# Kernel optimization log

Measured on AMD Instinct MI355X. Metric: run time of the kernel, lower is better.

The kernel has to match this reference:

```python
import jax, jax.numpy as jnp
import numpy as np

B, L, V, E, D, NH, HD, NL = 4, 2048, 32000, 300, 128, 4, 128, 3
D2 = NH * HD  # 512
W = 3  # ring window size (unfold_size)
EPS = 1e-5


def setup_inputs() -> dict:
    key = jax.random.key(0)
    ks = jax.random.split(key, 16)
    s = 0.02
    w = lambda k, shape: (jax.random.normal(k, shape, jnp.float32) * s)
    inp = {
        "tokens": jax.random.randint(ks[0], (B, L), 0, V),
        "mask": jax.random.randint(ks[1], (B, L), 0, 2).astype(jnp.int32),
        "emb_table": w(ks[2], (V, E)),
        "proj_w": w(ks[3], (D, E)),
        "proj_b": jnp.zeros((D,), jnp.float32),
        "ng": jnp.ones((NL, D), jnp.float32),
        "nb": jnp.zeros((NL, D), jnp.float32),
        "rq_w": w(ks[4], (NL, D2, D)), "rq_b": jnp.zeros((NL, D2), jnp.float32),
        "rk_w": w(ks[5], (NL, D2, D)), "rk_b": jnp.zeros((NL, D2), jnp.float32),
        "rv_w": w(ks[6], (NL, D2, D)), "rv_b": jnp.zeros((NL, D2), jnp.float32),
        "ro_w": w(ks[7], (NL, D, D2)), "ro_b": jnp.zeros((NL, D), jnp.float32),
        "sq_w": w(ks[8], (NL, D2, D)), "sq_b": jnp.zeros((NL, D2), jnp.float32),
        "sk_w": w(ks[9], (NL, D2, D)), "sk_b": jnp.zeros((NL, D2), jnp.float32),
        "sv_w": w(ks[10], (NL, D2, D)), "sv_b": jnp.zeros((NL, D2), jnp.float32),
        "so_w": w(ks[11], (NL, D, D2)), "so_b": jnp.zeros((NL, D), jnp.float32),
    }
    return inp


def _layernorm(x, g, b):
    mu = x.mean(-1, keepdims=True)
    var = x.var(-1, keepdims=True)
    return (x - mu) / jnp.sqrt(var + EPS) * g + b


def reference(tokens, mask, emb_table, proj_w, proj_b, ng, nb,
              rq_w, rq_b, rk_w, rk_b, rv_w, rv_b, ro_w, ro_b,
              sq_w, sq_b, sk_w, sk_b, sv_w, sv_b, so_w, so_b):
    b, l = tokens.shape
    pad = (mask == 0)                                        # [B,L] True at padding
    smask = jnp.concatenate([jnp.zeros((b, 1), bool), pad], axis=1)  # [B,L+1]
    x = emb_table[tokens] @ proj_w.T + proj_b                # [B,L,D]
    nodes = x
    relay = x.mean(axis=1)                                   # [B,D]
    r_embs = x                                               # fixed original embeddings
    scale = 1.0 / np.sqrt(HD).astype(np.float32)
    for i in range(NL):
        nx = _layernorm(nodes, ng[i], nb[i])
        # ----- MSA1: ring (windowed) attention + relay extras -----
        q = (nx @ rq_w[i].T + rq_b[i]).reshape(b, l, NH, HD)
        k = (nx @ rk_w[i].T + rk_b[i]).reshape(b, l, NH, HD)
        v = (nx @ rv_w[i].T + rv_b[i]).reshape(b, l, NH, HD)
        relay_bc = jnp.broadcast_to(relay[:, None, :], (b, l, D))
        ax = jnp.stack([r_embs, relay_bc], axis=2)           # [B,L,2,D]
        ak = (ax @ rk_w[i].T + rk_b[i]).reshape(b, l, 2, NH, HD)
        av = (ax @ rv_w[i].T + rv_b[i]).reshape(b, l, 2, NH, HD)
        kp = jnp.pad(k, ((0, 0), (1, 1), (0, 0), (0, 0)))    # zero pad like F.unfold
        vp = jnp.pad(v, ((0, 0), (1, 1), (0, 0), (0, 0)))
        kw = jnp.stack([kp[:, u:u + l] for u in range(W)], axis=2)  # [B,L,3,NH,HD]
        vw = jnp.stack([vp[:, u:u + l] for u in range(W)], axis=2)
        kall = jnp.concatenate([kw, ak], axis=2)             # [B,L,5,NH,HD]
        vall = jnp.concatenate([vw, av], axis=2)
        scores = jnp.einsum('blnh,blunh->blun', q, kall) * scale
        alphas = jax.nn.softmax(scores, axis=2)
        att = jnp.einsum('blun,blunh->blnh', alphas, vall).reshape(b, l, D2)
        nodes = nodes + jax.nn.leaky_relu(att @ ro_w[i].T + ro_b[i])
        # ----- MSA2: relay (global) attention over [relay; nodes] -----
        y = jnp.concatenate([relay[:, None, :], nodes], axis=1)      # [B,L+1,D]
        sq = (relay @ sq_w[i].T + sq_b[i]).reshape(b, NH, HD)
        sk = (y @ sk_w[i].T + sk_b[i]).reshape(b, l + 1, NH, HD)
        sv = (y @ sv_w[i].T + sv_b[i]).reshape(b, l + 1, NH, HD)
        pre = jnp.einsum('bnh,blnh->bnl', sq, sk) * scale            # [B,NH,L+1]
        pre = jnp.where(smask[:, None, :], -jnp.inf, pre)
        al = jax.nn.softmax(pre, axis=2)
        satt = jnp.einsum('bnl,blnh->bnh', al, sv).reshape(b, D2)
        relay = jax.nn.leaky_relu(satt @ so_w[i].T + so_b[i])
        nodes = jnp.where(pad[:, :, None], 0.0, nodes)
    return relay  # a_v: [B, d_model] (use_attention=False path)
```

## Files before the change

### kernel.cpp

```cpp
#include <hip/hip_runtime.h>
#include <hip/hip_bf16.h>

constexpr int B = 4, L = 2048, E = 300, D = 128, NH = 4, HD = 128, NL = 3, D2 = 512;
constexpr float EPS = 1e-5f;
constexpr float SCALE = 0.08838834764831843f;
constexpr int NCH = 64;

typedef unsigned int uint_t;
typedef unsigned short u16;
typedef short bf16x8 __attribute__((ext_vector_type(8)));
typedef float f32x4 __attribute__((ext_vector_type(4)));

__device__ __forceinline__ u16 f2bf(float f) {
  union { float f; uint_t i; } x; x.f = f;
  uint_t r = x.i + 0x7fffu + ((x.i >> 16) & 1u);
  return (u16)(r >> 16);
}
__device__ __forceinline__ uint_t packbf(float a, float b) {
  return (uint_t)f2bf(a) | ((uint_t)f2bf(b) << 16);
}
__device__ __forceinline__ float bf2f(u16 u) {
  union { uint_t i; float f; } x; x.i = ((uint_t)u) << 16; return x.f;
}
__device__ __forceinline__ float2 bf2x2(uint_t u) {
  union { uint_t i; float f; } a, b;
  a.i = (u & 0xffffu) << 16; b.i = u & 0xffff0000u;
  return make_float2(a.f, b.f);
}
struct f8 { float v[8]; };
__device__ __forceinline__ f8 unpack8(uint4 u) {
  f8 r;
  float2 a = bf2x2(u.x); r.v[0] = a.x; r.v[1] = a.y;
  float2 b = bf2x2(u.y); r.v[2] = b.x; r.v[3] = b.y;
  float2 c = bf2x2(u.z); r.v[4] = c.x; r.v[5] = c.y;
  float2 d = bf2x2(u.w); r.v[6] = d.x; r.v[7] = d.y;
  return r;
}

struct WCArgs { const float* s[4]; u16* d[4]; };
__global__ __launch_bounds__(256) void wconv(WCArgs wa) {
  int ti = blockIdx.y;
  const float* s = wa.s[ti]; u16* dd = wa.d[ti];
  int i = (blockIdx.x * 256 + threadIdx.x) * 4;
  float4 f = *(const float4*)(s + i);
  *(uint2*)(dd + i) = make_uint2(packbf(f.x, f.y), packbf(f.z, f.w));
}

struct GDesc { const u16* A; const u16* W; const float* bias; u16* outb; };
struct GArgs { GDesc d[5]; };

__global__ __launch_bounds__(256) void gemm_qkv(GArgs ga, int nby, int N) {
  __shared__ u16 As[128][136];
  __shared__ u16 Ws[128][136];
  int t = threadIdx.x;
  int bm = blockIdx.x;
  int di = blockIdx.y / nby, bn = blockIdx.y - di * nby;
  GDesc d = ga.d[di];
  const int rowA = bm * 128, rowW = bn * 128;

  f32x4 acc[4][4];
#pragma unroll
  for (int i = 0; i < 4; i++)
#pragma unroll
    for (int j = 0; j < 4; j++)
      acc[i][j] = (f32x4){0.f, 0.f, 0.f, 0.f};

  const int r = t >> 1, c0 = (t & 1) * 64;
  const int wid = t >> 6;
  const int wm = (wid & 1) * 64, wn = (wid >> 1) * 64;
  const int lr = t & 15, quad = (t >> 4) & 3;

  const u16* Arow = d.A + (size_t)(rowA + r) * 128;
  const u16* Wrow = d.W + (size_t)(rowW + r) * 128;
  uint4 av_[8], wv_[8];
#pragma unroll
  for (int i = 0; i < 8; i++) {
    av_[i] = *(const uint4*)(Arow + c0 + i * 8);
    wv_[i] = *(const uint4*)(Wrow + c0 + i * 8);
  }
#pragma unroll
  for (int i = 0; i < 8; i++) {
    *(uint4*)&As[r][c0 + i * 8] = av_[i];
    *(uint4*)&Ws[r][c0 + i * 8] = wv_[i];
  }
  __syncthreads();
#pragma unroll
  for (int ks = 0; ks < 4; ks++) {
    bf16x8 af[4], bfr[4];
#pragma unroll
    for (int mt = 0; mt < 4; mt++)
      af[mt] = *(const bf16x8*)&As[wm + mt * 16 + lr][ks * 32 + quad * 8];
#pragma unroll
    for (int nt = 0; nt < 4; nt++)
      bfr[nt] = *(const bf16x8*)&Ws[wn + nt * 16 + lr][ks * 32 + quad * 8];
#pragma unroll
    for (int mt = 0; mt < 4; mt++)
#pragma unroll
      for (int nt = 0; nt < 4; nt++)
        acc[mt][nt] = __builtin_amdgcn_mfma_f32_16x16x32_bf16(af[mt], bfr[nt], acc[mt][nt], 0, 0, 0);
  }
  __syncthreads();
#pragma unroll
  for (int nt = 0; nt < 4; nt++) {
    int colL = wn + nt * 16 + lr;
    float bv = d.bias[rowW + colL];
#pragma unroll
    for (int mt = 0; mt < 4; mt++) {
#pragma unroll
      for (int rr = 0; rr < 4; rr++) {
        int rowL = wm + mt * 16 + quad * 4 + rr;
        As[rowL][colL] = f2bf(acc[mt][nt][rr] + bv);
      }
    }
  }
  __syncthreads();
#pragma unroll
  for (int rep = 0; rep < 8; rep++) {
    int lin = rep * 256 + t;
    int rowL = lin >> 4, colL = (lin & 15) * 8;
    uint4 v = *(const uint4*)&As[rowL][colL];
    *(uint4*)&d.outb[(size_t)(rowA + rowL) * N + rowW + colL] = v;
  }
}

__global__ __launch_bounds__(256) void gemm_embed_ln(
    const float* __restrict__ emb, const float* __restrict__ W,
    const float* __restrict__ bias, const int* __restrict__ gather,
    const float* __restrict__ lng, const float* __restrict__ lnb,
    float* __restrict__ nodes, u16* __restrict__ xb, u16* __restrict__ nxb,
    float* __restrict__ relay) {
  __shared__ u16 As[64][72];
  __shared__ u16 Ws[128][72];
  __shared__ float C[64][132];
  __shared__ float gb[2][D];
  __shared__ float lmu[64], lrs[64];
  int t = threadIdx.x;
  int bm = blockIdx.x;
  const int rowA0 = bm * 64;

  f32x4 acc[2][4];
#pragma unroll
  for (int i = 0; i < 2; i++)
#pragma unroll
    for (int j = 0; j < 4; j++)
      acc[i][j] = (f32x4){0.f, 0.f, 0.f, 0.f};

  const int wid = t >> 6;
  const int wm = (wid & 1) * 32, wn = (wid >> 1) * 64;
  const int lr = t & 15, quad = (t >> 4) & 3;
  const int ra = t >> 2, ca = (t & 3) * 16;
  const int rw = t >> 1, cw = (t & 1) * 32;

  if (t < D) { gb[0][t] = lng[t]; gb[1][t] = lnb[t]; }

  const float* Arow = emb + (size_t)gather[rowA0 + ra] * E;
  const float* Wrow = W + (size_t)rw * E;

  for (int kt = 0; kt < E; kt += 64) {
    __syncthreads();
    bool full = (kt + 64 <= E);
#pragma unroll
    for (int ch = 0; ch < 4; ch++) {
      int c = kt + ca + ch * 4;
      float4 fa;
      if (full) fa = *(const float4*)(Arow + c);
      else {
        fa.x = (c + 0 < E) ? Arow[c + 0] : 0.f;
        fa.y = (c + 1 < E) ? Arow[c + 1] : 0.f;
        fa.z = (c + 2 < E) ? Arow[c + 2] : 0.f;
        fa.w = (c + 3 < E) ? Arow[c + 3] : 0.f;
      }
      *(uint2*)&As[ra][ca + ch * 4] = make_uint2(packbf(fa.x, fa.y), packbf(fa.z, fa.w));
    }
#pragma unroll
    for (int ch = 0; ch < 8; ch++) {
      int c = kt + cw + ch * 4;
      float4 fw;
      if (full) fw = *(const float4*)(Wrow + c);
      else {
        fw.x = (c + 0 < E) ? Wrow[c + 0] : 0.f;
        fw.y = (c + 1 < E) ? Wrow[c + 1] : 0.f;
        fw.z = (c + 2 < E) ? Wrow[c + 2] : 0.f;
        fw.w = (c + 3 < E) ? Wrow[c + 3] : 0.f;
      }
      *(uint2*)&Ws[rw][cw + ch * 4] = make_uint2(packbf(fw.x, fw.y), packbf(fw.z, fw.w));
    }
    __syncthreads();
#pragma unroll
    for (int ks = 0; ks < 2; ks++) {
      bf16x8 af[2], bfr[4];
#pragma unroll
      for (int mt = 0; mt < 2; mt++)
        af[mt] = *(const bf16x8*)&As[wm + mt * 16 + lr][ks * 32 + quad * 8];
#pragma unroll
      for (int nt = 0; nt < 4; nt++)
        bfr[nt] = *(const bf16x8*)&Ws[wn + nt * 16 + lr][ks * 32 + quad * 8];
#pragma unroll
      for (int mt = 0; mt < 2; mt++)
#pragma unroll
        for (int nt = 0; nt < 4; nt++)
          acc[mt][nt] = __builtin_amdgcn_mfma_f32_16x16x32_bf16(af[mt], bfr[nt], acc[mt][nt], 0, 0, 0);
    }
  }
#pragma unroll
  for (int nt = 0; nt < 4; nt++) {
    int col = wn + nt * 16 + lr;
    float bv = bias[col];
#pragma unroll
    for (int mt = 0; mt < 2; mt++) {
#pragma unroll
      for (int rr = 0; rr < 4; rr++) {
        int row = wm + mt * 16 + quad * 4 + rr;
        C[row][col] = acc[mt][nt][rr] + bv;
      }
    }
  }
  __syncthreads();
  if (t < 64) {
    float s = 0.f, s2 = 0.f;
#pragma unroll 16
    for (int j = 0; j < D; j++) { float v = C[t][j]; s += v; s2 += v * v; }
    float mu = s * (1.0f / D);
    float var = s2 * (1.0f / D) - mu * mu;
    lmu[t] = mu; lrs[t] = rsqrtf(var + EPS);
  }
  __syncthreads();
#pragma unroll
  for (int rep = 0; rep < 8; rep++) {
    int lin = rep * 1024 + t * 4;
    int row = lin >> 7, col = lin & 127;
    float4 v = *(const float4*)&C[row][col];
    size_t g = (size_t)(rowA0 + row) * D + col;
    *(float4*)&nodes[g] = v;
    *(uint2*)&xb[g] = make_uint2(packbf(v.x, v.y), packbf(v.z, v.w));
    float mu = lmu[row], rs = lrs[row];
    float o0 = (v.x - mu) * rs * gb[0][col] + gb[1][col];
    float o1 = (v.y - mu) * rs * gb[0][col + 1] + gb[1][col + 1];
    float o2 = (v.z - mu) * rs * gb[0][col + 2] + gb[1][col + 2];
    float o3 = (v.w - mu) * rs * gb[0][col + 3] + gb[1][col + 3];
    *(uint2*)&nxb[g] = make_uint2(packbf(o0, o1), packbf(o2, o3));
  }
  if (t < D) {
    int b = rowA0 >> 11;
    float s = 0.f;
#pragma unroll 16
    for (int r2 = 0; r2 < 64; r2++) s += C[r2][t];
    atomicAdd(&relay[b * D + t], s * (1.0f / L));
  }
}

__global__ __launch_bounds__(256) void gemm_ro_ln(
    const u16* __restrict__ A,
    const u16* __restrict__ W,
    const float* __restrict__ bias,
    const int* __restrict__ mask,
    const float* __restrict__ lng, const float* __restrict__ lnb,
    const float* __restrict__ uvec, const float* __restrict__ cvec,
    float* __restrict__ nodes, u16* __restrict__ nxb,
    float* __restrict__ pm, float* __restrict__ ps, float* __restrict__ pw,
    int do_ln) {
  __shared__ u16 As[32][136];
  __shared__ u16 Ws[128][136];
  __shared__ float C[32][132];
  __shared__ float gb[2][D];
  __shared__ float lmu[32], lrs[32];
  __shared__ float usv[NH][D];
  __shared__ float cv2[NH];
  __shared__ float scs[NH][32];
  __shared__ float esr[NH][32];
  int t = threadIdx.x;
  int bm = blockIdx.x;
  const int rowA0 = bm * 32;
  const int b4 = rowA0 >> 11;
  const int chunk = (rowA0 >> 5) & 63;

  f32x4 acc[4];
#pragma unroll
  for (int j = 0; j < 4; j++) acc[j] = (f32x4){0.f, 0.f, 0.f, 0.f};

  const int wid = t >> 6;
  const int wm = (wid & 1) * 16, wn = (wid >> 1) * 64;
  const int lr = t & 15, quad = (t >> 4) & 3;
  const int ra = t >> 3, ca = (t & 7) * 16;
  const int rw = t >> 1, cw = (t & 1) * 64;

  if (do_ln && t < D) { gb[0][t] = lng[t]; gb[1][t] = lnb[t]; }
#pragma unroll
  for (int rep = 0; rep < 2; rep++) {
    int idx = rep * 256 + t;
    usv[idx >> 7][idx & 127] = uvec[(size_t)b4 * NH * D + idx];
  }
  if (t < NH) cv2[t] = cvec[b4 * NH + t];

  const u16* Arow = A + (size_t)(rowA0 + ra) * 512;
  const u16* Wrow = W + (size_t)rw * 512;

  for (int kt = 0; kt < 512; kt += 128) {
    uint4 a0 = *(const uint4*)(Arow + kt + ca);
    uint4 a1 = *(const uint4*)(Arow + kt + ca + 8);
    uint4 w0 = *(const uint4*)(Wrow + kt + cw);
    uint4 w1 = *(const uint4*)(Wrow + kt + cw + 8);
    uint4 w2 = *(const uint4*)(Wrow + kt + cw + 16);
    uint4 w3 = *(const uint4*)(Wrow + kt + cw + 24);
    uint4 w4 = *(const uint4*)(Wrow + kt + cw + 32);
    uint4 w5 = *(const uint4*)(Wrow + kt + cw + 40);
    uint4 w6 = *(const uint4*)(Wrow + kt + cw + 48);
    uint4 w7 = *(const uint4*)(Wrow + kt + cw + 56);
    __syncthreads();
    *(uint4*)&As[ra][ca] = a0; *(uint4*)&As[ra][ca + 8] = a1;
    *(uint4*)&Ws[rw][cw] = w0; *(uint4*)&Ws[rw][cw + 8] = w1;
    *(uint4*)&Ws[rw][cw + 16] = w2; *(uint4*)&Ws[rw][cw + 24] = w3;
    *(uint4*)&Ws[rw][cw + 32] = w4; *(uint4*)&Ws[rw][cw + 40] = w5;
    *(uint4*)&Ws[rw][cw + 48] = w6; *(uint4*)&Ws[rw][cw + 56] = w7;
    __syncthreads();
#pragma unroll
    for (int ks = 0; ks < 4; ks++) {
      bf16x8 af = *(const bf16x8*)&As[wm + lr][ks * 32 + quad * 8];
      bf16x8 bfr[4];
#pragma unroll
      for (int nt = 0; nt < 4; nt++)
        bfr[nt] = *(const bf16x8*)&Ws[wn + nt * 16 + lr][ks * 32 + quad * 8];
#pragma unroll
      for (int nt = 0; nt < 4; nt++)
        acc[nt] = __builtin_amdgcn_mfma_f32_16x16x32_bf16(af, bfr[nt], acc[nt], 0, 0, 0);
    }
  }
  __syncthreads();
#pragma unroll
  for (int nt = 0; nt < 4; nt++) {
    int col = wn + nt * 16 + lr;
    float bv = bias[col];
#pragma unroll
    for (int rr = 0; rr < 4; rr++) {
      int row = wm + quad * 4 + rr;
      float v = acc[nt][rr] + bv;
      v = (v > 0.f) ? v : 0.01f * v;
      v += nodes[(size_t)(rowA0 + row) * D + col];
      if (mask[rowA0 + row] == 0) v = 0.f;
      C[row][col] = v;
    }
  }
  __syncthreads();
  if (t < 32) {
    float s = 0.f, s2 = 0.f;
#pragma unroll 16
    for (int j = 0; j < D; j++) { float v = C[t][j]; s += v; s2 += v * v; }
    float mu = s * (1.0f / D);
    float var = s2 * (1.0f / D) - mu * mu;
    lmu[t] = mu; lrs[t] = rsqrtf(var + EPS);
  }
  __syncthreads();
#pragma unroll
  for (int rep = 0; rep < 4; rep++) {
    int lin = rep * 1024 + t * 4;
    int row = lin >> 7, col = lin & 127;
    float4 v = *(const float4*)&C[row][col];
    size_t g = (size_t)(rowA0 + row) * D + col;
    *(float4*)&nodes[g] = v;
    if (do_ln) {
      float mu = lmu[row], rs = lrs[row];
      float o0 = (v.x - mu) * rs * gb[0][col] + gb[1][col];
      float o1 = (v.y - mu) * rs * gb[0][col + 1] + gb[1][col + 1];
      float o2 = (v.z - mu) * rs * gb[0][col + 2] + gb[1][col + 2];
      float o3 = (v.w - mu) * rs * gb[0][col + 3] + gb[1][col + 3];
      *(uint2*)&nxb[g] = make_uint2(packbf(o0, o1), packbf(o2, o3));
    }
  }
  {
    int n = wid, lane = t & 63;
    int bn = b4 * NH + n;
    const float2* un = (const float2*)usv[n];
    float2 uv2 = un[lane];
    for (int r2 = 0; r2 < 32; r2++) {
      float2 cc = ((const float2*)&C[r2][0])[lane];
      float p = uv2.x * cc.x + uv2.y * cc.y;
#pragma unroll
      for (int o = 1; o < 64; o <<= 1) p += __shfl_xor(p, o, 64);
      if (lane == 0) {
        float s = p + cv2[n];
        if (mask[rowA0 + r2] == 0) s = -1e30f;
        scs[n][r2] = s;
      }
    }
    float m = -1e30f;
    for (int r2 = 0; r2 < 32; r2++) m = fmaxf(m, scs[n][r2]);
    if (lane < 32) esr[n][lane] = expf(scs[n][lane] - m);
    float sum = 0.f;
    for (int r2 = 0; r2 < 32; r2++) sum += esr[n][r2];
    if (lane == 0) { pm[bn * NCH + chunk] = m; ps[bn * NCH + chunk] = sum; }
    float a0 = 0.f, a1 = 0.f;
    for (int r2 = 0; r2 < 32; r2++) {
      float e = esr[n][r2];
      float2 cc = ((const float2*)&C[r2][0])[lane];
      a0 += e * cc.x; a1 += e * cc.y;
    }
    float* pwp = pw + ((size_t)bn * NCH + chunk) * D + 2 * lane;
    pwp[0] = a0; pwp[1] = a1;
  }
}

__device__ __forceinline__ void do_relay_proj(
    int b, int di, int t, const float* rel,
    const float* rkw, const float* rkb, const float* rvw, const float* rvb,
    const float* sqw, const float* sqb, const float* skw, const float* skb_,
    float* relay_k, float* relay_v, float* u, float* cvec,
    float* sql, float* cred) {
  const float4* r4 = (const float4*)rel;
  if (di < 8) {
    int which = di >> 2;
    int n = (di & 3) * 128 + t;
    const float* W = which ? rvw : rkw;
    float acc = (which ? rvb : rkb)[n];
    const float4* w4 = (const float4*)(W + (size_t)n * D);
#pragma unroll 8
    for (int i = 0; i < D / 4; i++) {
      float4 w = w4[i], r = r4[i];
      acc += w.x * r.x + w.y * r.y + w.z * r.z + w.w * r.w;
    }
    (which ? relay_v : relay_k)[(size_t)b * D2 + n] = acc;
  } else {
    int n = di - 8;
    {
      int nh = n * HD + t;
      float acc = sqb[nh];
      const float4* w4 = (const float4*)(sqw + (size_t)nh * D);
#pragma unroll 8
      for (int i = 0; i < D / 4; i++) {
        float4 w = w4[i], r = r4[i];
        acc += w.x * r.x + w.y * r.y + w.z * r.z + w.w * r.w;
      }
      sql[t] = acc;
    }
    __syncthreads();
    {
      float cp = sql[t] * skb_[n * HD + t];
#pragma unroll
      for (int o = 1; o < 64; o <<= 1) cp += __shfl_xor(cp, o, 64);
      if ((t & 63) == 0) cred[t >> 6] = cp;
    }
    float a0 = 0.f, a1 = 0.f, a2 = 0.f, a3 = 0.f;
    const float* wp = skw + (size_t)(n * HD) * D + t;
    for (int h = 0; h < HD; h += 4) {
      a0 += sql[h] * wp[(size_t)h * D];
      a1 += sql[h + 1] * wp[(size_t)(h + 1) * D];
      a2 += sql[h + 2] * wp[(size_t)(h + 2) * D];
      a3 += sql[h + 3] * wp[(size_t)(h + 3) * D];
    }
    u[((size_t)b * NH + n) * D + t] = (a0 + a1 + a2 + a3) * SCALE;
    __syncthreads();
    if (t == 0) cvec[b * NH + n] = (cred[0] + cred[1]) * SCALE;
  }
}

__global__ __launch_bounds__(128) void relay_proj(
    const float* __restrict__ relay,
    const float* __restrict__ rkw, const float* __restrict__ rkb,
    const float* __restrict__ rvw, const float* __restrict__ rvb,
    const float* __restrict__ sqw, const float* __restrict__ sqb,
    const float* __restrict__ skw, const float* __restrict__ skb_,
    float* __restrict__ relay_k, float* __restrict__ relay_v,
    float* __restrict__ u, float* __restrict__ cvec) {
  __shared__ float rel[D];
  __shared__ float sql[HD];
  __shared__ float cred[2];
  int b = blockIdx.x, di = blockIdx.y, t = threadIdx.x;
  rel[t] = relay[(size_t)b * D + t];
  __syncthreads();
  do_relay_proj(b, di, t, rel, rkw, rkb, rvw, rvb, sqw, sqb, skw, skb_,
                relay_k, relay_v, u, cvec, sql, cred);
}

__global__ __launch_bounds__(256) void ring_attn_kernel(
    const u16* __restrict__ q, const u16* __restrict__ k, const u16* __restrict__ v,
    const u16* __restrict__ akr, const u16* __restrict__ avr,
    const float* __restrict__ rk, const float* __restrict__ rv,
    u16* __restrict__ att) {
  int wv = threadIdx.x >> 6, lane = threadIdx.x & 63;
  int bl = blockIdx.x * 4 + wv;
  int b = bl >> 11, l = bl & (L - 1);
  size_t rowoff = (size_t)bl * D2 + lane * 8;

  uint4 qd = *(const uint4*)(q + rowoff);
  uint4 kd[5], vd[5];
  bool valid[3];
#pragma unroll
  for (int u = 0; u < 3; u++) {
    int ll = l + u - 1;
    valid[u] = (ll >= 0 && ll < L);
    size_t off = ((size_t)b * L + ll) * D2 + lane * 8;
    if (valid[u]) { kd[u] = *(const uint4*)(k + off); vd[u] = *(const uint4*)(v + off); }
    else { kd[u] = make_uint4(0, 0, 0, 0); vd[u] = make_uint4(0, 0, 0, 0); }
  }
  kd[3] = *(const uint4*)(akr + rowoff);
  vd[3] = *(const uint4*)(avr + rowoff);
  size_t rb = (size_t)b * D2 + lane * 8;
  float4 rk0 = *(const float4*)(rk + rb), rk1 = *(const float4*)(rk + rb + 4);
  float4 rv0 = *(const float4*)(rv + rb), rv1 = *(const float4*)(rv + rb + 4);

  f8 qf = unpack8(qd);
  f8 kf[5], vf[5];
#pragma unroll
  for (int u = 0; u < 4; u++) { kf[u] = unpack8(kd[u]); vf[u] = unpack8(vd[u]); }
  kf[4].v[0] = rk0.x; kf[4].v[1] = rk0.y; kf[4].v[2] = rk0.z; kf[4].v[3] = rk0.w;
  kf[4].v[4] = rk1.x; kf[4].v[5] = rk1.y; kf[4].v[6] = rk1.z; kf[4].v[7] = rk1.w;
  vf[4].v[0] = rv0.x; vf[4].v[1] = rv0.y; vf[4].v[2] = rv0.z; vf[4].v[3] = rv0.w;
  vf[4].v[4] = rv1.x; vf[4].v[5] = rv1.y; vf[4].v[6] = rv1.z; vf[4].v[7] = rv1.w;

  float s[5];
#pragma unroll
  for (int u = 0; u < 5; u++) {
    float p = 0.f;
#pragma unroll
    for (int j = 0; j < 8; j++) p += qf.v[j] * kf[u].v[j];
#pragma unroll
    for (int o = 1; o < 16; o <<= 1) p += __shfl_xor(p, o, 64);
    s[u] = p * SCALE;
  }
  float m = s[0];
#pragma unroll
  for (int u = 1; u < 5; u++) m = fmaxf(m, s[u]);
  float e[5], sum = 0.f;
#pragma unroll
  for (int u = 0; u < 5; u++) { e[u] = expf(s[u] - m); sum += e[u]; }
  float inv = 1.0f / sum;
  float o[8];
#pragma unroll
  for (int j = 0; j < 8; j++) {
    float a = 0.f;
#pragma unroll
    for (int u = 0; u < 5; u++) a += e[u] * vf[u].v[j];
    o[j] = a * inv;
  }
  uint4 od;
  od.x = packbf(o[0], o[1]); od.y = packbf(o[2], o[3]);
  od.z = packbf(o[4], o[5]); od.w = packbf(o[6], o[7]);
  *(uint4*)(att + rowoff) = od;
}

__global__ __launch_bounds__(128) void relay_final(
    const float* __restrict__ pm, const float* __restrict__ ps, const float* __restrict__ pw,
    const float* __restrict__ relay_entry,
    const float* __restrict__ uvec_in, const float* __restrict__ cvec_in,
    const float* __restrict__ svw, const float* __restrict__ svb,
    const float* __restrict__ sow, const float* __restrict__ sob,
    const float* __restrict__ nrkw, const float* __restrict__ nrkb,
    const float* __restrict__ nrvw, const float* __restrict__ nrvb,
    const float* __restrict__ nsqw, const float* __restrict__ nsqb,
    const float* __restrict__ nskw, const float* __restrict__ nskb,
    float* __restrict__ relay_out,
    float* __restrict__ relay_k, float* __restrict__ relay_v,
    float* __restrict__ u_out, float* __restrict__ cvec_out, int do_proj) {
  int b = blockIdx.x, di = blockIdx.y, t = threadIdx.x;
  __shared__ float uu[NH][D];
  __shared__ float rel0[D];
  __shared__ float pms[NH][NCH], pss[NH][NCH], ecs[NH][NCH];
  __shared__ float s0s[NH], cvs[NH];
  __shared__ float wsum[NH][D];
  __shared__ float satts[D2];
  __shared__ float rel[D];
  __shared__ float sql[HD];
  __shared__ float cred[2];

  rel0[t] = relay_entry[(size_t)b * D + t];
#pragma unroll
  for (int rep = 0; rep < 4; rep++) {
    int idx = rep * 128 + t;
    uu[idx >> 7][idx & 127] = uvec_in[(size_t)b * NH * D + idx];
  }
  if (t < NH) cvs[t] = cvec_in[b * NH + t];
#pragma unroll
  for (int rep = 0; rep < 2; rep++) {
    int idx = rep * 128 + t;
    int n = idx >> 6, c = idx & 63;
    pms[n][c] = pm[(b * NH + n) * NCH + c];
    pss[n][c] = ps[(b * NH + n) * NCH + c];
  }
  __syncthreads();
  int g = t >> 5, lt = t & 31;
  {
    float p = 0.f;
#pragma unroll
    for (int kk = 0; kk < 4; kk++) { int j = lt * 4 + kk; p += uu[g][j] * rel0[j]; }
#pragma unroll
    for (int o = 1; o < 32; o <<= 1) p += __shfl_xor(p, o, 64);
    if (lt == 0) s0s[g] = p + cvs[g];
  }
  __syncthreads();
  float s0 = s0s[g];
  float M = s0;
  for (int c = 0; c < NCH; c++) M = fmaxf(M, pms[g][c]);
  for (int c = lt; c < NCH; c += 32) ecs[g][c] = expf(pms[g][c] - M);
  __syncthreads();
  float e0 = expf(s0 - M);
  float S = e0;
  for (int c = 0; c < NCH; c++) S += pss[g][c] * ecs[g][c];
  float invS = 1.0f / S;
#pragma unroll
  for (int kk = 0; kk < 4; kk++) {
    int h = lt * 4 + kk;
    float acc = e0 * rel0[h];
    const float* pwp = pw + ((size_t)(b * NH + g) * NCH) * D + h;
    for (int c = 0; c < NCH; c++) acc += ecs[g][c] * pwp[(size_t)c * D];
    wsum[g][h] = acc * invS;
  }
  __syncthreads();
#pragma unroll
  for (int rep = 0; rep < 4; rep++) {
    int nh = rep * 128 + t;
    int hn = nh >> 7;
    float acc = svb[nh];
    const float4* wp = (const float4*)(svw + (size_t)nh * D);
    const float4* wl = (const float4*)wsum[hn];
#pragma unroll 8
    for (int d = 0; d < D / 4; d++) {
      float4 a = wl[d], wv4 = wp[d];
      acc += a.x * wv4.x + a.y * wv4.y + a.z * wv4.z + a.w * wv4.w;
    }
    satts[nh] = acc;
  }
  __syncthreads();
  {
    float acc = sob[t];
    const float4* wp = (const float4*)(sow + (size_t)t * D2);
    const float4* a4 = (const float4*)satts;
#pragma unroll 8
    for (int j = 0; j < D2 / 4; j++) {
      float4 a = a4[j], wv4 = wp[j];
      acc += a.x * wv4.x + a.y * wv4.y + a.z * wv4.z + a.w * wv4.w;
    }
    acc = (acc > 0.f) ? acc : 0.01f * acc;
    rel[t] = acc;
    relay_out[(size_t)b * D + t] = acc;
  }
  __syncthreads();
  if (do_proj)
    do_relay_proj(b, di, t, rel, nrkw, nrkb, nrvw, nrvb, nsqw, nsqb, nskw, nskb,
                  relay_k, relay_v, u_out, cvec_out, sql, cred);
}

extern "C" void kernel_launch(void* const* d_in, const int* in_sizes, int n_in,
                              void* d_out, int out_size, void* d_ws, size_t ws_size,
                              hipStream_t stream) {
  const int* tokens = (const int*)d_in[0];
  const int* mask = (const int*)d_in[1];
  const float* emb = (const float*)d_in[2];
  const float* proj_w = (const float*)d_in[3];
  const float* proj_b = (const float*)d_in[4];
  const float* ng = (const float*)d_in[5];
  const float* nb = (const float*)d_in[6];
  const float* rq_w = (const float*)d_in[7], * rq_b = (const float*)d_in[8];
  const float* rk_w = (const float*)d_in[9], * rk_b = (const float*)d_in[10];
  const float* rv_w = (const float*)d_in[11], * rv_b = (const float*)d_in[12];
  const float* ro_w = (const float*)d_in[13], * ro_b = (const float*)d_in[14];
  const float* sq_w = (const float*)d_in[15], * sq_b = (const float*)d_in[16];
  const float* sk_w = (const float*)d_in[17], * sk_b = (const float*)d_in[18];
  const float* sv_w = (const float*)d_in[19], * sv_b = (const float*)d_in[20];
  const float* so_w = (const float*)d_in[21], * so_b = (const float*)d_in[22];

  const size_t BLD = (size_t)B * L * D;
  const size_t BLD4 = (size_t)B * L * D2;
  const size_t WTEN = (size_t)NL * D * D2;

  float* fp = (float*)d_ws;
  float* nodes = fp;                    fp += BLD;
  float* rbuf0 = fp;                    fp += B * D;
  float* rbuf1 = fp;                    fp += B * D;
  float* relay_k = fp;                  fp += B * D2;
  float* relay_v = fp;                  fp += B * D2;
  float* uv0 = fp;                      fp += B * NH * D;
  float* uv1 = fp;                      fp += B * NH * D;
  float* cv0 = fp;                      fp += B * NH;
  float* cv1 = fp;                      fp += B * NH;
  float* pm = fp;                       fp += B * NH * NCH;
  float* ps = fp;                       fp += B * NH * NCH;
  float* pw = fp;                       fp += (size_t)B * NH * NCH * D;
  u16* up = (u16*)fp;
  u16* xb = up;                         up += BLD;
  u16* nxb = up;                        up += BLD;
  u16* qb = up;                         up += BLD4;
  u16* kb = up;                         up += BLD4;
  u16* vb = up;                         up += BLD4;
  u16* akb = up;                        up += BLD4;
  u16* avb = up;                        up += BLD4;
  u16* attb = up;                       up += BLD4;
  u16* wb = up;
  u16* wrq = wb, * wrk = wb + WTEN, * wrv = wb + 2 * WTEN, * wro = wb + 3 * WTEN;

  float* rbuf[2] = {rbuf0, rbuf1};
  float* uv[2] = {uv0, uv1};
  float* cv[2] = {cv0, cv1};

  hipMemsetAsync(rbuf0, 0, B * D * sizeof(float), stream);

  {
    WCArgs wa;
    wa.s[0] = rq_w; wa.s[1] = rk_w; wa.s[2] = rv_w; wa.s[3] = ro_w;
    wa.d[0] = wrq; wa.d[1] = wrk; wa.d[2] = wrv; wa.d[3] = wro;
    wconv<<<dim3(WTEN / 1024, 4), 256, 0, stream>>>(wa);
  }
  gemm_embed_ln<<<128, 256, 0, stream>>>(emb, proj_w, proj_b, tokens, ng, nb,
                                         nodes, xb, nxb, rbuf0);
  relay_proj<<<dim3(B, 12), 128, 0, stream>>>(rbuf0, rk_w, rk_b, rv_w, rv_b, sq_w, sq_b,
                                              sk_w, sk_b, relay_k, relay_v, uv0, cv0);

  for (int i = 0; i < NL; i++) {
    const size_t wo = (size_t)i * D * D2;
    const float* rqbi = rq_b + (size_t)i * D2;
    const float* rkbi = rk_b + (size_t)i * D2;
    const float* rvbi = rv_b + (size_t)i * D2;
    const float* robi = ro_b + (size_t)i * D;
    const float* svwi = sv_w + wo, * svbi = sv_b + (size_t)i * D2;
    const float* sowi = so_w + wo, * sobi = so_b + (size_t)i * D;
    const int e = i & 1, nx2 = e ^ 1;
    const int last = (i == NL - 1);

    {
      GArgs ga = {};
      ga.d[0] = {nxb, wrq + wo, rqbi, qb};
      ga.d[1] = {nxb, wrk + wo, rkbi, kb};
      ga.d[2] = {nxb, wrv + wo, rvbi, vb};
      ga.d[3] = {xb,  wrk + wo, rkbi, akb};
      ga.d[4] = {xb,  wrv + wo, rvbi, avb};
      gemm_qkv<<<dim3(64, 20), 256, 0, stream>>>(ga, 4, D2);
    }
    ring_attn_kernel<<<B * L / 4, 256, 0, stream>>>(qb, kb, vb, akb, avb, relay_k, relay_v, attb);
    gemm_ro_ln<<<256, 256, 0, stream>>>(
        attb, wro + wo, robi, mask,
        last ? nullptr : ng + (i + 1) * D, last ? nullptr : nb + (i + 1) * D,
        uv[e], cv[e], nodes, nxb, pm, ps, pw, last ? 0 : 1);
    const size_t wn_ = (size_t)(i + 1) * D * D2;
    float* relay_dst = last ? (float*)d_out : rbuf[nx2];
    relay_final<<<dim3(B, last ? 1 : 12), 128, 0, stream>>>(
        pm, ps, pw, rbuf[e], uv[e], cv[e], svwi, svbi, sowi, sobi,
        last ? nullptr : rk_w + wn_, last ? nullptr : rk_b + (size_t)(i + 1) * D2,
        last ? nullptr : rv_w + wn_, last ? nullptr : rv_b + (size_t)(i + 1) * D2,
        last ? nullptr : sq_w + wn_, last ? nullptr : sq_b + (size_t)(i + 1) * D2,
        last ? nullptr : sk_w + wn_, last ? nullptr : sk_b + (size_t)(i + 1) * D2,
        relay_dst, relay_k, relay_v, uv[nx2], cv[nx2], last ? 0 : 1);
  }
}
```

Before: 387.5 us.

## Fold relay projections into QKV GEMM launch and slim relay combine kernel

Moves the per-layer relay key/value/query projection work out of the relay-final kernel and the initial standalone launch, and runs it as 24 extra blocks prepended to the QKV GEMM grid. The relay combine kernel becomes a single 512-thread block per batch with wider parallel reductions, and no longer holds the projection stage serially at its tail. The aim is to remove one kernel launch plus a serialized low-parallelism tail per layer by overlapping the small projections with the GEMM. The u/c buffers are no longer double-buffered, which relies on stream ordering between the combine kernel and the next GEMM.

Result: faster. 361.4 us (-6.7%).

```diff
diff --git a/kernel.cpp b/kernel.cpp
--- a/kernel.cpp
+++ b/kernel.cpp
@@ -48,13 +48,77 @@
 
 struct GDesc { const u16* A; const u16* W; const float* bias; u16* outb; };
 struct GArgs { GDesc d[5]; };
-
-__global__ __launch_bounds__(256) void gemm_qkv(GArgs ga, int nby, int N) {
+struct PArgs {
+  const float* rel;
+  const float* rkw; const float* rkb;
+  const float* rvw; const float* rvb;
+  const float* sqw; const float* sqb;
+  const float* skw; const float* skb;
+  float* relay_k; float* relay_v;
+  float* u; float* cvec;
+};
+constexpr int NPROJ = 24;
+
+__global__ __launch_bounds__(256) void gemm_qkv(GArgs ga, PArgs pa, int N) {
+  int bid = blockIdx.x;
+  int t = threadIdx.x;
+  if (bid < NPROJ) {
+    __shared__ float rel[D];
+    __shared__ float sql2[2][HD];
+    __shared__ float credp[4];
+    int b = bid / 6, j = bid % 6;
+    if (t < D) rel[t] = pa.rel[(size_t)b * D + t];
+    __syncthreads();
+    const float4* r4 = (const float4*)rel;
+    if (j < 4) {
+      int which = j >> 1;
+      int n = (j & 1) * 256 + t;
+      const float* W = which ? pa.rvw : pa.rkw;
+      float acc = (which ? pa.rvb : pa.rkb)[n];
+      const float4* w4 = (const float4*)(W + (size_t)n * D);
+#pragma unroll 8
+      for (int i = 0; i < D / 4; i++) {
+        float4 w = w4[i], r = r4[i];
+        acc += w.x * r.x + w.y * r.y + w.z * r.z + w.w * r.w;
+      }
+      (which ? pa.relay_v : pa.relay_k)[(size_t)b * D2 + n] = acc;
+    } else {
+      int hh = t >> 7, th = t & 127;
+      int n = (j - 4) * 2 + hh;
+      int nh = n * HD + th;
+      float acc = pa.sqb[nh];
+      const float4* w4 = (const float4*)(pa.sqw + (size_t)nh * D);
+#pragma unroll 8
+      for (int i = 0; i < D / 4; i++) {
+        float4 w = w4[i], r = r4[i];
+        acc += w.x * r.x + w.y * r.y + w.z * r.z + w.w * r.w;
+      }
+      sql2[hh][th] = acc;
+      __syncthreads();
+      float cp = acc * pa.skb[nh];
+#pragma unroll
+      for (int o = 1; o < 64; o <<= 1) cp += __shfl_xor(cp, o, 64);
+      if ((t & 63) == 0) credp[t >> 6] = cp;
+      float a0 = 0.f, a1 = 0.f, a2 = 0.f, a3 = 0.f;
+      const float* wp = pa.skw + (size_t)(n * HD) * D + th;
+      for (int hx = 0; hx < HD; hx += 4) {
+        a0 += sql2[hh][hx] * wp[(size_t)hx * D];
+        a1 += sql2[hh][hx + 1] * wp[(size_t)(hx + 1) * D];
+        a2 += sql2[hh][hx + 2] * wp[(size_t)(hx + 2) * D];
+        a3 += sql2[hh][hx + 3] * wp[(size_t)(hx + 3) * D];
+      }
+      pa.u[((size_t)b * NH + n) * D + th] = (a0 + a1 + a2 + a3) * SCALE;
+      __syncthreads();
+      if (th == 0) pa.cvec[b * NH + n] = (credp[2 * hh] + credp[2 * hh + 1]) * SCALE;
+    }
+    return;
+  }
   __shared__ u16 As[128][136];
   __shared__ u16 Ws[128][136];
-  int t = threadIdx.x;
-  int bm = blockIdx.x;
-  int di = blockIdx.y / nby, bn = blockIdx.y - di * nby;
+  int g = bid - NPROJ;
+  int bm = g & 63;
+  int y = g >> 6;
+  int di = y >> 2, bn = y & 3;
   GDesc d = ga.d[di];
   const int rowA = bm * 128, rowW = bn * 128;
 
@@ -399,77 +463,6 @@
   }
 }
 
-__device__ __forceinline__ void do_relay_proj(
-    int b, int di, int t, const float* rel,
-    const float* rkw, const float* rkb, const float* rvw, const float* rvb,
-    const float* sqw, const float* sqb, const float* skw, const float* skb_,
-    float* relay_k, float* relay_v, float* u, float* cvec,
-    float* sql, float* cred) {
-  const float4* r4 = (const float4*)rel;
-  if (di < 8) {
-    int which = di >> 2;
-    int n = (di & 3) * 128 + t;
-    const float* W = which ? rvw : rkw;
-    float acc = (which ? rvb : rkb)[n];
-    const float4* w4 = (const float4*)(W + (size_t)n * D);
-#pragma unroll 8
-    for (int i = 0; i < D / 4; i++) {
-      float4 w = w4[i], r = r4[i];
-      acc += w.x * r.x + w.y * r.y + w.z * r.z + w.w * r.w;
-    }
-    (which ? relay_v : relay_k)[(size_t)b * D2 + n] = acc;
-  } else {
-    int n = di - 8;
-    {
-      int nh = n * HD + t;
-      float acc = sqb[nh];
-      const float4* w4 = (const float4*)(sqw + (size_t)nh * D);
-#pragma unroll 8
-      for (int i = 0; i < D / 4; i++) {
-        float4 w = w4[i], r = r4[i];
-        acc += w.x * r.x + w.y * r.y + w.z * r.z + w.w * r.w;
-      }
-      sql[t] = acc;
-    }
-    __syncthreads();
-    {
-      float cp = sql[t] * skb_[n * HD + t];
-#pragma unroll
-      for (int o = 1; o < 64; o <<= 1) cp += __shfl_xor(cp, o, 64);
-      if ((t & 63) == 0) cred[t >> 6] = cp;
-    }
-    float a0 = 0.f, a1 = 0.f, a2 = 0.f, a3 = 0.f;
-    const float* wp = skw + (size_t)(n * HD) * D + t;
-    for (int h = 0; h < HD; h += 4) {
-      a0 += sql[h] * wp[(size_t)h * D];
-      a1 += sql[h + 1] * wp[(size_t)(h + 1) * D];
-      a2 += sql[h + 2] * wp[(size_t)(h + 2) * D];
-      a3 += sql[h + 3] * wp[(size_t)(h + 3) * D];
-    }
-    u[((size_t)b * NH + n) * D + t] = (a0 + a1 + a2 + a3) * SCALE;
-    __syncthreads();
-    if (t == 0) cvec[b * NH + n] = (cred[0] + cred[1]) * SCALE;
-  }
-}
-
-__global__ __launch_bounds__(128) void relay_proj(
-    const float* __restrict__ relay,
-    const float* __restrict__ rkw, const float* __restrict__ rkb,
-    const float* __restrict__ rvw, const float* __restrict__ rvb,
-    const float* __restrict__ sqw, const float* __restrict__ sqb,
-    const float* __restrict__ skw, const float* __restrict__ skb_,
-    float* __restrict__ relay_k, float* __restrict__ relay_v,
-    float* __restrict__ u, float* __restrict__ cvec) {
-  __shared__ float rel[D];
-  __shared__ float sql[HD];
-  __shared__ float cred[2];
-  int b = blockIdx.x, di = blockIdx.y, t = threadIdx.x;
-  rel[t] = relay[(size_t)b * D + t];
-  __syncthreads();
-  do_relay_proj(b, di, t, rel, rkw, rkb, rvw, rvb, sqw, sqb, skw, skb_,
-                relay_k, relay_v, u, cvec, sql, cred);
-}
-
 __global__ __launch_bounds__(256) void ring_attn_kernel(
     const u16* __restrict__ q, const u16* __restrict__ k, const u16* __restrict__ v,
     const u16* __restrict__ akr, const u16* __restrict__ avr,
@@ -537,105 +530,80 @@
   *(uint4*)(att + rowoff) = od;
 }
 
-__global__ __launch_bounds__(128) void relay_final(
-    const float* __restrict__ pm, const float* __restrict__ ps, const float* __restrict__ pw,
+__global__ __launch_bounds__(512) void relay_combine(
+    const float* __restrict__ pm, const float* __restrict__ ps,
+    const float* __restrict__ pw,
     const float* __restrict__ relay_entry,
     const float* __restrict__ uvec_in, const float* __restrict__ cvec_in,
     const float* __restrict__ svw, const float* __restrict__ svb,
     const float* __restrict__ sow, const float* __restrict__ sob,
-    const float* __restrict__ nrkw, const float* __restrict__ nrkb,
-    const float* __restrict__ nrvw, const float* __restrict__ nrvb,
-    const float* __restrict__ nsqw, const float* __restrict__ nsqb,
-    const float* __restrict__ nskw, const float* __restrict__ nskb,
-    float* __restrict__ relay_out,
-    float* __restrict__ relay_k, float* __restrict__ relay_v,
-    float* __restrict__ u_out, float* __restrict__ cvec_out, int do_proj) {
-  int b = blockIdx.x, di = blockIdx.y, t = threadIdx.x;
-  __shared__ float uu[NH][D];
+    float* __restrict__ relay_out) {
   __shared__ float rel0[D];
-  __shared__ float pms[NH][NCH], pss[NH][NCH], ecs[NH][NCH];
-  __shared__ float s0s[NH], cvs[NH];
+  __shared__ float wpart[8];
+  __shared__ float ecs[NH][NCH];
   __shared__ float wsum[NH][D];
   __shared__ float satts[D2];
-  __shared__ float rel[D];
-  __shared__ float sql[HD];
-  __shared__ float cred[2];
-
-  rel0[t] = relay_entry[(size_t)b * D + t];
-#pragma unroll
-  for (int rep = 0; rep < 4; rep++) {
-    int idx = rep * 128 + t;
-    uu[idx >> 7][idx & 127] = uvec_in[(size_t)b * NH * D + idx];
-  }
-  if (t < NH) cvs[t] = cvec_in[b * NH + t];
-#pragma unroll
-  for (int rep = 0; rep < 2; rep++) {
-    int idx = rep * 128 + t;
-    int n = idx >> 6, c = idx & 63;
-    pms[n][c] = pm[(b * NH + n) * NCH + c];
-    pss[n][c] = ps[(b * NH + n) * NCH + c];
-  }
-  __syncthreads();
-  int g = t >> 5, lt = t & 31;
+  __shared__ float rred[4][D];
+  int b = blockIdx.x, t = threadIdx.x;
+  int n = t >> 7, h = t & 127;
+  int w = t >> 6, lane = t & 63;
+  if (t < D) rel0[t] = relay_entry[(size_t)b * D + t];
+  __syncthreads();
+  float p = uvec_in[((size_t)b * NH + n) * D + h] * rel0[h];
+#pragma unroll
+  for (int o = 1; o < 64; o <<= 1) p += __shfl_xor(p, o, 64);
+  if (lane == 0) wpart[w] = p;
+  __syncthreads();
+  float s0 = wpart[2 * n] + wpart[2 * n + 1] + cvec_in[b * NH + n];
+  int c = h & 63;
+  float pmv = pm[(b * NH + n) * NCH + c];
+  float m = fmaxf(pmv, s0);
+#pragma unroll
+  for (int o = 1; o < 64; o <<= 1) m = fmaxf(m, __shfl_xor(m, o, 64));
+  float ec = expf(pmv - m);
+  if (h < 64) ecs[n][h] = ec;
+  float sc = ps[(b * NH + n) * NCH + c] * ec;
+#pragma unroll
+  for (int o = 1; o < 64; o <<= 1) sc += __shfl_xor(sc, o, 64);
+  float e0 = expf(s0 - m);
+  float invS = 1.0f / (e0 + sc);
+  __syncthreads();
+  float acc = e0 * rel0[h];
+  const float* pwp = pw + ((size_t)(b * NH + n) * NCH) * D + h;
+#pragma unroll 8
+  for (int cc = 0; cc < NCH; cc++) acc += ecs[n][cc] * pwp[(size_t)cc * D];
+  wsum[n][h] = acc * invS;
+  __syncthreads();
   {
-    float p = 0.f;
-#pragma unroll
-    for (int kk = 0; kk < 4; kk++) { int j = lt * 4 + kk; p += uu[g][j] * rel0[j]; }
-#pragma unroll
-    for (int o = 1; o < 32; o <<= 1) p += __shfl_xor(p, o, 64);
-    if (lt == 0) s0s[g] = p + cvs[g];
-  }
-  __syncthreads();
-  float s0 = s0s[g];
-  float M = s0;
-  for (int c = 0; c < NCH; c++) M = fmaxf(M, pms[g][c]);
-  for (int c = lt; c < NCH; c += 32) ecs[g][c] = expf(pms[g][c] - M);
-  __syncthreads();
-  float e0 = expf(s0 - M);
-  float S = e0;
-  for (int c = 0; c < NCH; c++) S += pss[g][c] * ecs[g][c];
-  float invS = 1.0f / S;
-#pragma unroll
-  for (int kk = 0; kk < 4; kk++) {
-    int h = lt * 4 + kk;
-    float acc = e0 * rel0[h];
-    const float* pwp = pw + ((size_t)(b * NH + g) * NCH) * D + h;
-    for (int c = 0; c < NCH; c++) acc += ecs[g][c] * pwp[(size_t)c * D];
-    wsum[g][h] = acc * invS;
-  }
-  __syncthreads();
-#pragma unroll
-  for (int rep = 0; rep < 4; rep++) {
-    int nh = rep * 128 + t;
-    int hn = nh >> 7;
-    float acc = svb[nh];
-    const float4* wp = (const float4*)(svw + (size_t)nh * D);
-    const float4* wl = (const float4*)wsum[hn];
+    float a = svb[t];
+    const float4* wp = (const float4*)(svw + (size_t)t * D);
+    const float4* wl = (const float4*)wsum[n];
 #pragma unroll 8
-    for (int d = 0; d < D / 4; d++) {
-      float4 a = wl[d], wv4 = wp[d];
-      acc += a.x * wv4.x + a.y * wv4.y + a.z * wv4.z + a.w * wv4.w;
-    }
-    satts[nh] = acc;
+    for (int dd = 0; dd < D / 4; dd++) {
+      float4 x = wl[dd], y = wp[dd];
+      a += x.x * y.x + x.y * y.y + x.z * y.z + x.w * y.w;
+    }
+    satts[t] = a;
   }
   __syncthreads();
   {
-    float acc = sob[t];
-    const float4* wp = (const float4*)(sow + (size_t)t * D2);
-    const float4* a4 = (const float4*)satts;
+    int part = t >> 7, col = t & 127;
+    float a = 0.f;
+    const float4* wp = (const float4*)(sow + (size_t)col * D2 + part * 128);
+    const float4* a4 = (const float4*)(satts + part * 128);
 #pragma unroll 8
-    for (int j = 0; j < D2 / 4; j++) {
-      float4 a = a4[j], wv4 = wp[j];
-      acc += a.x * wv4.x + a.y * wv4.y + a.z * wv4.z + a.w * wv4.w;
-    }
-    acc = (acc > 0.f) ? acc : 0.01f * acc;
-    rel[t] = acc;
-    relay_out[(size_t)b * D + t] = acc;
-  }
-  __syncthreads();
-  if (do_proj)
-    do_relay_proj(b, di, t, rel, nrkw, nrkb, nrvw, nrvb, nsqw, nsqb, nskw, nskb,
-                  relay_k, relay_v, u_out, cvec_out, sql, cred);
+    for (int jj = 0; jj < 32; jj++) {
+      float4 x = a4[jj], y = wp[jj];
+      a += x.x * y.x + x.y * y.y + x.z * y.z + x.w * y.w;
+    }
+    rred[part][col] = a;
+  }
+  __syncthreads();
+  if (t < D) {
+    float a = sob[t] + rred[0][t] + rred[1][t] + rred[2][t] + rred[3][t];
+    a = (a > 0.f) ? a : 0.01f * a;
+    relay_out[(size_t)b * D + t] = a;
+  }
 }
 
 extern "C" void kernel_launch(void* const* d_in, const int* in_sizes, int n_in,
@@ -667,10 +635,8 @@
   float* rbuf1 = fp;                    fp += B * D;
   float* relay_k = fp;                  fp += B * D2;
   float* relay_v = fp;                  fp += B * D2;
-  float* uv0 = fp;                      fp += B * NH * D;
-  float* uv1 = fp;                      fp += B * NH * D;
-  float* cv0 = fp;                      fp += B * NH;
-  float* cv1 = fp;                      fp += B * NH;
+  float* uv = fp;                       fp += B * NH * D;
+  float* cv = fp;                       fp += B * NH;
   float* pm = fp;                       fp += B * NH * NCH;
   float* ps = fp;                       fp += B * NH * NCH;
   float* pw = fp;                       fp += (size_t)B * NH * NCH * D;
@@ -686,10 +652,6 @@
   u16* wb = up;
   u16* wrq = wb, * wrk = wb + WTEN, * wrv = wb + 2 * WTEN, * wro = wb + 3 * WTEN;
 
-  float* rbuf[2] = {rbuf0, rbuf1};
-  float* uv[2] = {uv0, uv1};
-  float* cv[2] = {cv0, cv1};
-
   hipMemsetAsync(rbuf0, 0, B * D * sizeof(float), stream);
 
   {
@@ -700,8 +662,9 @@
   }
   gemm_embed_ln<<<128, 256, 0, stream>>>(emb, proj_w, proj_b, tokens, ng, nb,
                                          nodes, xb, nxb, rbuf0);
-  relay_proj<<<dim3(B, 12), 128, 0, stream>>>(rbuf0, rk_w, rk_b, rv_w, rv_b, sq_w, sq_b,
-                                              sk_w, sk_b, relay_k, relay_v, uv0, cv0);
+
+  float* rin[3] = {rbuf0, rbuf1, rbuf0};
+  float* rout[3] = {rbuf1, rbuf0, (float*)d_out};
 
   for (int i = 0; i < NL; i++) {
     const size_t wo = (size_t)i * D * D2;
@@ -711,7 +674,6 @@
     const float* robi = ro_b + (size_t)i * D;
     const float* svwi = sv_w + wo, * svbi = sv_b + (size_t)i * D2;
     const float* sowi = so_w + wo, * sobi = so_b + (size_t)i * D;
-    const int e = i & 1, nx2 = e ^ 1;
     const int last = (i == NL - 1);
 
     {
@@ -721,21 +683,21 @@
       ga.d[2] = {nxb, wrv + wo, rvbi, vb};
       ga.d[3] = {xb,  wrk + wo, rkbi, akb};
       ga.d[4] = {xb,  wrv + wo, rvbi, avb};
-      gemm_qkv<<<dim3(64, 20), 256, 0, stream>>>(ga, 4, D2);
+      PArgs pa;
+      pa.rel = rin[i];
+      pa.rkw = rk_w + wo; pa.rkb = rkbi;
+      pa.rvw = rv_w + wo; pa.rvb = rvbi;
+      pa.sqw = sq_w + wo; pa.sqb = sq_b + (size_t)i * D2;
+      pa.skw = sk_w + wo; pa.skb = sk_b + (size_t)i * D2;
+      pa.relay_k = relay_k; pa.relay_v = relay_v; pa.u = uv; pa.cvec = cv;
+      gemm_qkv<<<64 * 20 + NPROJ, 256, 0, stream>>>(ga, pa, D2);
     }
     ring_attn_kernel<<<B * L / 4, 256, 0, stream>>>(qb, kb, vb, akb, avb, relay_k, relay_v, attb);
     gemm_ro_ln<<<256, 256, 0, stream>>>(
         attb, wro + wo, robi, mask,
         last ? nullptr : ng + (i + 1) * D, last ? nullptr : nb + (i + 1) * D,
-        uv[e], cv[e], nodes, nxb, pm, ps, pw, last ? 0 : 1);
-    const size_t wn_ = (size_t)(i + 1) * D * D2;
-    float* relay_dst = last ? (float*)d_out : rbuf[nx2];
-    relay_final<<<dim3(B, last ? 1 : 12), 128, 0, stream>>>(
-        pm, ps, pw, rbuf[e], uv[e], cv[e], svwi, svbi, sowi, sobi,
-        last ? nullptr : rk_w + wn_, last ? nullptr : rk_b + (size_t)(i + 1) * D2,
-        last ? nullptr : rv_w + wn_, last ? nullptr : rv_b + (size_t)(i + 1) * D2,
-        last ? nullptr : sq_w + wn_, last ? nullptr : sq_b + (size_t)(i + 1) * D2,
-        last ? nullptr : sk_w + wn_, last ? nullptr : sk_b + (size_t)(i + 1) * D2,
-        relay_dst, relay_k, relay_v, uv[nx2], cv[nx2], last ? 0 : 1);
-  }
-}
+        uv, cv, nodes, nxb, pm, ps, pw, last ? 0 : 1);
+    relay_combine<<<B, 512, 0, stream>>>(pm, ps, pw, rin[i], uv, cv,
+                                         svwi, svbi, sowi, sobi, rout[i]);
+  }
+}
```
